# Kernel tuning notes

Measured on AMD Instinct MI355X. Metric: run time of the kernel, lower is better.

## Reference

```python
import jax, jax.numpy as jnp
import numpy as np

NUM_LAYERS = 3

def setup_inputs() -> dict:
    key = jax.random.key(0)
    k1, k2, k3, k4 = jax.random.split(key, 4)
    N, D, E = 100000, 128, 3200000
    x = jax.random.normal(k1, (N, D), dtype=jnp.float32)
    edge_row = jax.random.randint(k2, (E,), 0, N, dtype=jnp.int64 if jax.config.jax_enable_x64 else jnp.int32)
    edge_col = jax.random.randint(k3, (E,), 0, N, dtype=jnp.int64 if jax.config.jax_enable_x64 else jnp.int32)
    # normalized-adjacency-like positive values
    edge_val = jax.random.uniform(k4, (E,), dtype=jnp.float32)
    return {"x": x, "edge_row": edge_row, "edge_col": edge_col, "edge_val": edge_val}

def _spmm(edge_row, edge_col, edge_val, emb, num_nodes):
    # out[r] += val * emb[c]  -- sparse adjacency @ emb
    msgs = edge_val[:, None] * emb[edge_col]          # [E, D] gather + scale
    return jax.ops.segment_sum(msgs, edge_row, num_segments=num_nodes)

def reference(x, edge_row, edge_col, edge_val):
    N = x.shape[0]
    emb = x
    acc = x  # running sum over layer embeddings (layer 0 included)
    for _ in range(NUM_LAYERS):
        emb = _spmm(edge_row, edge_col, edge_val, emb, N)
        acc = acc + emb
    # mean over (num_layers + 1) stacked embeddings, without materializing the stack
    return acc / jnp.float32(NUM_LAYERS + 1)
```

## Files before the change

### kernel.cpp

```cpp
#include <hip/hip_runtime.h>

#define DIMS 128
#define RPB 64
#define CAP 3072
#define NBK_MAX 1600
#define NBINS 1024
#define NBANDS 13
#define RPW 16

typedef _Float16 half_t;
typedef _Float16 half2_t __attribute__((ext_vector_type(2)));
typedef unsigned short ushort_t;

static __device__ __forceinline__ unsigned halfbits(float v) {
    half_t h = (half_t)v;
    unsigned short us;
    __builtin_memcpy(&us, &h, 2);
    return (unsigned)us;
}
static __device__ __forceinline__ half2_t h2(int b) { return __builtin_bit_cast(half2_t, b); }
static __device__ __forceinline__ int ih(half2_t h) { return __builtin_bit_cast(int, h); }

__global__ void cvt_kernel(const float* __restrict__ src, half_t* __restrict__ dst, int n2) {
    int i = blockIdx.x * blockDim.x + threadIdx.x;
    if (i >= n2) return;
    float2 v = reinterpret_cast<const float2*>(src)[i];
    half2_t h;
    h.x = (half_t)v.x;
    h.y = (half_t)v.y;
    reinterpret_cast<half2_t*>(&dst[0])[i] = h;
}

__global__ __launch_bounds__(512) void binA_kernel(
    const int* __restrict__ row, const int* __restrict__ col,
    const float* __restrict__ val, int E, int nbk,
    int* __restrict__ fill, int2* __restrict__ staged) {
    __shared__ int cnt[NBK_MAX];
    __shared__ int base[NBK_MAX];
    const int t = threadIdx.x;
    const int tile0 = blockIdx.x * 8192;
    for (int j = t; j < nbk; j += 512) cnt[j] = 0;
    __syncthreads();
    for (int k = 0; k < 4; ++k) {
        int e = tile0 + (k * 512 + t) * 4;
        if (e + 3 < E) {
            int4 r4 = *reinterpret_cast<const int4*>(&row[e]);
            atomicAdd(&cnt[r4.x >> 6], 1);
            atomicAdd(&cnt[r4.y >> 6], 1);
            atomicAdd(&cnt[r4.z >> 6], 1);
            atomicAdd(&cnt[r4.w >> 6], 1);
        } else {
            for (int j = e; j < E; ++j) atomicAdd(&cnt[row[j] >> 6], 1);
        }
    }
    __syncthreads();
    for (int j = t; j < nbk; j += 512) {
        int c = cnt[j];
        base[j] = c ? atomicAdd(&fill[j], c) : 0;
        cnt[j] = 0;
    }
    __syncthreads();
    for (int k = 0; k < 4; ++k) {
        int e = tile0 + (k * 512 + t) * 4;
        int n = (e + 3 < E) ? 4 : max(0, E - e);
        if (n == 4) {
            int4 r4 = *reinterpret_cast<const int4*>(&row[e]);
            int4 c4 = *reinterpret_cast<const int4*>(&col[e]);
            float4 v4 = *reinterpret_cast<const float4*>(&val[e]);
            int rr[4] = {r4.x, r4.y, r4.z, r4.w};
            int cc[4] = {c4.x, c4.y, c4.z, c4.w};
            float vv[4] = {v4.x, v4.y, v4.z, v4.w};
#pragma unroll
            for (int j = 0; j < 4; ++j) {
                int b = rr[j] >> 6;
                int p = base[b] + atomicAdd(&cnt[b], 1);
                if (p < CAP) {
                    unsigned hb = halfbits(vv[j]);
                    int2 pk;
                    pk.x = (int)(((unsigned)(rr[j] & 63) << 26) | ((unsigned)cc[j] << 8));
                    pk.y = (int)((hb << 16) | hb);
                    staged[(size_t)b * CAP + p] = pk;
                }
            }
        } else {
            for (int j = e; j < e + n; ++j) {
                int r = row[j];
                int b = r >> 6;
                int p = base[b] + atomicAdd(&cnt[b], 1);
                if (p < CAP) {
                    unsigned hb = halfbits(val[j]);
                    int2 pk;
                    pk.x = (int)(((unsigned)(r & 63) << 26) | ((unsigned)col[j] << 8));
                    pk.y = (int)((hb << 16) | hb);
                    staged[(size_t)b * CAP + p] = pk;
                }
            }
        }
    }
}

__global__ __launch_bounds__(512) void sort_bucket(
    const int* __restrict__ fill, int2* __restrict__ staged,
    ushort_t* __restrict__ binoff) {
    __shared__ int2 outb[CAP];
    __shared__ int cur[NBINS];
    __shared__ int wsum[8];
    const int b = blockIdx.x;
    const int t = threadIdx.x;
    const int w = t >> 6, lane = t & 63;
    const int cnt = min(fill[b], CAP);
    int2* gb = staged + (size_t)b * CAP;

    cur[2 * t] = 0;
    cur[2 * t + 1] = 0;
    __syncthreads();
    for (int i = t; i < cnt; i += 512) {
        unsigned k = (unsigned)gb[i].x;
        int key = (int)((k >> 26) << 4) | (int)((k >> 21) & 0xF);
        atomicAdd(&cur[key], 1);
    }
    __syncthreads();
    int h0 = cur[2 * t], h1 = cur[2 * t + 1];
    int s = h0 + h1;
    int v = s;
    for (int d = 1; d < 64; d <<= 1) {
        int u = __shfl_up(v, d, 64);
        if (lane >= d) v += u;
    }
    if (lane == 63) wsum[w] = v;
    __syncthreads();
    if (t < 8) {
        int ws = wsum[t];
        int vv = ws;
        for (int d = 1; d < 8; d <<= 1) {
            int u = __shfl_up(vv, d, 64);
            if (t >= d) vv += u;
        }
        wsum[t] = vv - ws;
    }
    __syncthreads();
    int excl = wsum[w] + (v - s);
    cur[2 * t] = excl;
    cur[2 * t + 1] = excl + h0;
    {
        ushort2 u2;
        u2.x = (ushort_t)excl;
        u2.y = (ushort_t)(excl + h0);
        reinterpret_cast<ushort2*>(binoff + (size_t)b * NBINS)[t] = u2;
    }
    __syncthreads();
    for (int i = t; i < cnt; i += 512) {
        int2 pk = gb[i];
        unsigned k = (unsigned)pk.x;
        int key = (int)((k >> 26) << 4) | (int)((k >> 21) & 0xF);
        int p = atomicAdd(&cur[key], 1);
        outb[p] = pk;
    }
    __syncthreads();
    for (int i = t; i < cnt; i += 512) gb[i] = outb[i];
}

template <int MODE>
__global__ __launch_bounds__(256, 7) void spmm_kernel(
    const half_t* __restrict__ emb_in, const ushort_t* __restrict__ binoff,
    const int2* __restrict__ staged, int N,
    half_t* __restrict__ emb_out, half_t* __restrict__ acc_h,
    float* __restrict__ out) {
    const int wid = (blockIdx.x * blockDim.x + threadIdx.x) >> 6;
    const int lane = threadIdx.x & 63;
    const int r0 = wid * RPW;
    if (r0 >= N) return;
    const int bucket = r0 >> 6;
    const int g = lane >> 4;
    const int l16 = lane & 15;
    const int gbase = g << 4;
    const unsigned q16 = (unsigned)l16 << 4;
    const int2* eb = staged + (size_t)bucket * CAP;
    const char* tbl = reinterpret_cast<const char*>(emb_in);
    const ushort_t* bo = binoff + (size_t)bucket * NBINS + (((r0 & 63) + (g << 2)) << 4);

    half2_t acc[4][4];
#pragma unroll
    for (int u = 0; u < 4; ++u)
#pragma unroll
        for (int s = 0; s < 4; ++s) acc[u][s] = (half2_t)0;

    int bs0 = (int)bo[0], bs1 = (int)bo[16], bs2 = (int)bo[32], bs3 = (int)bo[48];

    for (int b = 0; b < NBANDS; ++b) {
#define ROW_BAND(RR, BSV)                                                     \
        {                                                                     \
            const int be = (int)bo[RR * 16 + b + 1];                          \
            for (int j0 = BSV; j0 < be; j0 += 16) {                           \
                const int2 myE = eb[min(j0 + l16, be - 1)];                   \
                const int cnt = min(16, be - j0);                             \
                for (int j = 0; j < cnt; ++j) {                               \
                    const int ex = __shfl(myE.x, gbase + j, 64);              \
                    const int ey = __shfl(myE.y, gbase + j, 64);              \
                    const unsigned voff = ((unsigned)ex & 0x03FFFF00u) + q16; \
                    const int4 t4 = *reinterpret_cast<const int4*>(tbl + voff); \
                    const half2_t vv = h2(ey);                                \
                    acc[RR][0] = h2(t4.x) * vv + acc[RR][0];                  \
                    acc[RR][1] = h2(t4.y) * vv + acc[RR][1];                  \
                    acc[RR][2] = h2(t4.z) * vv + acc[RR][2];                  \
                    acc[RR][3] = h2(t4.w) * vv + acc[RR][3];                  \
                }                                                             \
            }                                                                 \
            BSV = be;                                                         \
        }
        ROW_BAND(0, bs0)
        ROW_BAND(1, bs1)
        ROW_BAND(2, bs2)
        ROW_BAND(3, bs3)
#undef ROW_BAND
    }

#pragma unroll
    for (int rr = 0; rr < 4; ++rr) {
        const int r = r0 + (g << 2) + rr;
        const size_t o = (size_t)r * DIMS + ((size_t)l16 << 3);
        const half2_t a0 = acc[rr][0], a1 = acc[rr][1];
        const half2_t a2 = acc[rr][2], a3 = acc[rr][3];
        if (MODE == 0 || MODE == 1) {
            *reinterpret_cast<int4*>(&emb_out[o]) = make_int4(ih(a0), ih(a1), ih(a2), ih(a3));
        }
        if (MODE == 0) {
            int4 xv = *reinterpret_cast<const int4*>(&emb_in[o]);
            *reinterpret_cast<int4*>(&acc_h[o]) = make_int4(
                ih(h2(xv.x) + a0), ih(h2(xv.y) + a1), ih(h2(xv.z) + a2), ih(h2(xv.w) + a3));
        } else if (MODE == 1) {
            int4 cv = *reinterpret_cast<const int4*>(&acc_h[o]);
            *reinterpret_cast<int4*>(&acc_h[o]) = make_int4(
                ih(h2(cv.x) + a0), ih(h2(cv.y) + a1), ih(h2(cv.z) + a2), ih(h2(cv.w) + a3));
        } else {
            int4 cv = *reinterpret_cast<const int4*>(&acc_h[o]);
            half2_t c0 = h2(cv.x), c1 = h2(cv.y), c2 = h2(cv.z), c3 = h2(cv.w);
            float4 f0 = make_float4(((float)c0.x + (float)a0.x) * 0.25f,
                                    ((float)c0.y + (float)a0.y) * 0.25f,
                                    ((float)c1.x + (float)a1.x) * 0.25f,
                                    ((float)c1.y + (float)a1.y) * 0.25f);
            float4 f1 = make_float4(((float)c2.x + (float)a2.x) * 0.25f,
                                    ((float)c2.y + (float)a2.y) * 0.25f,
                                    ((float)c3.x + (float)a3.x) * 0.25f,
                                    ((float)c3.y + (float)a3.y) * 0.25f);
            float4* po = reinterpret_cast<float4*>(&out[o]);
            po[0] = f0;
            po[1] = f1;
        }
    }
}


extern "C" void kernel_launch(void* const* d_in, const int* in_sizes, int n_in,
                              void* d_out, int out_size, void* d_ws, size_t ws_size,
                              hipStream_t stream) {
    const float* x = (const float*)d_in[0];
    const int* erow = (const int*)d_in[1];
    const int* ecol = (const int*)d_in[2];
    const float* eval = (const float*)d_in[3];
    const int N = in_sizes[0] / DIMS;
    const int E = in_sizes[1];
    float* out = (float*)d_out;
    const int nbk = (N + RPB - 1) / RPB;

    char* ws = (char*)d_ws;
    size_t off = 0;
    auto carve = [&](size_t bytes) {
        void* p = ws + off;
        off = (off + bytes + 255) & ~(size_t)255;
        return p;
    };
    half_t* xh = (half_t*)carve((size_t)N * DIMS * sizeof(half_t));
    half_t* embB1 = (half_t*)carve((size_t)N * DIMS * sizeof(half_t));
    half_t* acc_h = (half_t*)carve((size_t)N * DIMS * sizeof(half_t));
    int2* staged = (int2*)carve((size_t)nbk * CAP * sizeof(int2));
    int* fill = (int*)carve((size_t)nbk * sizeof(int));
    ushort_t* binoff = (ushort_t*)carve((size_t)nbk * NBINS * sizeof(ushort_t));
    (void)ws_size;

    hipMemsetAsync(fill, 0, (size_t)nbk * sizeof(int), stream);
    const int n2 = N * DIMS / 2;
    cvt_kernel<<<(n2 + 255) / 256, 256, 0, stream>>>(x, xh, n2);
    binA_kernel<<<(E + 8191) / 8192, 512, 0, stream>>>(erow, ecol, eval, E, nbk, fill, staged);
    sort_bucket<<<nbk, 512, 0, stream>>>(fill, staged, binoff);

    const int waves = (N + RPW - 1) / RPW;
    const int spmm_blocks = (waves + 3) / 4;
    spmm_kernel<0><<<spmm_blocks, 256, 0, stream>>>(xh, binoff, staged, N, embB1, acc_h, out);
    spmm_kernel<1><<<spmm_blocks, 256, 0, stream>>>(embB1, binoff, staged, N, xh, acc_h, out);
    spmm_kernel<2><<<spmm_blocks, 256, 0, stream>>>(xh, binoff, staged, N, embB1, acc_h, out);
}
```

Baseline: 588.0 us.

## Interleave four rows per band to issue independent gathers, dropping shuffles

Replaces the per-row sequential edge loop, which staged edges through cross-lane shuffles, with a band loop that walks all four rows together. Each lane loads its edge directly from the staged buffer and issues four independent 16-byte gathers before doing the FMAs, which raises memory-level parallelism. In exchange, rows shorter than the band's longest row do padded iterations with zero weight and redundant loads, and the many scalar edge loads replace the coalesced shuffle scheme.

```diff
diff --git a/kernel.cpp b/kernel.cpp
--- a/kernel.cpp
+++ b/kernel.cpp
@@ -173,7 +173,6 @@
     const int bucket = r0 >> 6;
     const int g = lane >> 4;
     const int l16 = lane & 15;
-    const int gbase = g << 4;
     const unsigned q16 = (unsigned)l16 << 4;
     const int2* eb = staged + (size_t)bucket * CAP;
     const char* tbl = reinterpret_cast<const char*>(emb_in);
@@ -185,34 +184,39 @@
 #pragma unroll
         for (int s = 0; s < 4; ++s) acc[u][s] = (half2_t)0;
 
-    int bs0 = (int)bo[0], bs1 = (int)bo[16], bs2 = (int)bo[32], bs3 = (int)bo[48];
-
-    for (int b = 0; b < NBANDS; ++b) {
-#define ROW_BAND(RR, BSV)                                                     \
-        {                                                                     \
-            const int be = (int)bo[RR * 16 + b + 1];                          \
-            for (int j0 = BSV; j0 < be; j0 += 16) {                           \
-                const int2 myE = eb[min(j0 + l16, be - 1)];                   \
-                const int cnt = min(16, be - j0);                             \
-                for (int j = 0; j < cnt; ++j) {                               \
-                    const int ex = __shfl(myE.x, gbase + j, 64);              \
-                    const int ey = __shfl(myE.y, gbase + j, 64);              \
-                    const unsigned voff = ((unsigned)ex & 0x03FFFF00u) + q16; \
-                    const int4 t4 = *reinterpret_cast<const int4*>(tbl + voff); \
-                    const half2_t vv = h2(ey);                                \
-                    acc[RR][0] = h2(t4.x) * vv + acc[RR][0];                  \
-                    acc[RR][1] = h2(t4.y) * vv + acc[RR][1];                  \
-                    acc[RR][2] = h2(t4.z) * vv + acc[RR][2];                  \
-                    acc[RR][3] = h2(t4.w) * vv + acc[RR][3];                  \
-                }                                                             \
-            }                                                                 \
-            BSV = be;                                                         \
-        }
-        ROW_BAND(0, bs0)
-        ROW_BAND(1, bs1)
-        ROW_BAND(2, bs2)
-        ROW_BAND(3, bs3)
-#undef ROW_BAND
+    int bs[4], be[4];
+#pragma unroll
+    for (int rr = 0; rr < 4; ++rr) bs[rr] = (int)bo[rr * 16];
+
+    for (int b = 1; b <= NBANDS; ++b) {
+#pragma unroll
+        for (int rr = 0; rr < 4; ++rr) be[rr] = (int)bo[rr * 16 + b];
+        const int mx = max(max(be[0] - bs[0], be[1] - bs[1]),
+                           max(be[2] - bs[2], be[3] - bs[3]));
+        for (int s = 0; s < mx; ++s) {
+            int2 e[4];
+#pragma unroll
+            for (int rr = 0; rr < 4; ++rr) {
+                int j = bs[rr] + min(s, be[rr] - bs[rr] - 1);
+                e[rr] = eb[max(j, 0)];
+            }
+            int4 t4[4];
+#pragma unroll
+            for (int rr = 0; rr < 4; ++rr) {
+                t4[rr] = *reinterpret_cast<const int4*>(
+                    tbl + (((unsigned)e[rr].x & 0x03FFFF00u) + q16));
+            }
+#pragma unroll
+            for (int rr = 0; rr < 4; ++rr) {
+                const half2_t vv = h2((s < be[rr] - bs[rr]) ? e[rr].y : 0);
+                acc[rr][0] = h2(t4[rr].x) * vv + acc[rr][0];
+                acc[rr][1] = h2(t4[rr].y) * vv + acc[rr][1];
+                acc[rr][2] = h2(t4[rr].z) * vv + acc[rr][2];
+                acc[rr][3] = h2(t4[rr].w) * vv + acc[rr][3];
+            }
+        }
+#pragma unroll
+        for (int rr = 0; rr < 4; ++rr) bs[rr] = be[rr];
     }
 
 #pragma unroll
```

After: 675.9 us. +15.0%, slower.
